# Kernel optimization log

Hardware: AMD Instinct MI355X
Metric: run time of the kernel (lower is better)

The kernel has to match this reference:

```python
import jax, jax.numpy as jnp
import numpy as np

EMBED_DIM = 1024
NUM_HEADS = 16
HEAD_DIM = EMBED_DIM // NUM_HEADS
SEQ = 2048
BSZ = 2


def setup_inputs() -> dict:
    key = jax.random.key(0)
    ks = jax.random.split(key, 12)
    f = jnp.float32
    query = jax.random.normal(ks[0], (SEQ, BSZ, EMBED_DIM), f)
    k_in = jax.random.normal(ks[1], (SEQ, BSZ, EMBED_DIM), f)
    v_in = jax.random.normal(ks[2], (SEQ, BSZ, EMBED_DIM), f)
    s = 0.02  # weight init scale
    q_w = jax.random.normal(ks[3], (EMBED_DIM, EMBED_DIM), f) * s
    q_b = jax.random.normal(ks[4], (EMBED_DIM,), f) * s
    k_w = jax.random.normal(ks[5], (EMBED_DIM, EMBED_DIM), f) * s
    k_b = jax.random.normal(ks[6], (EMBED_DIM,), f) * s
    v_w = jax.random.normal(ks[7], (EMBED_DIM, EMBED_DIM), f) * s
    v_b = jax.random.normal(ks[8], (EMBED_DIM,), f) * s
    o_w_mean = jax.random.normal(ks[9], (EMBED_DIM, EMBED_DIM), f) * s
    # lgstd ~ uniform(2*log(stdv), log(stdv)) with stdv = 1/sqrt(out+1)
    stdv = 1.0 / np.sqrt(EMBED_DIM + 1)
    o_w_lgstd = jax.random.uniform(ks[10], (EMBED_DIM, EMBED_DIM), f,
                                   2.0 * np.log(stdv), np.log(stdv))
    eps = jax.random.normal(ks[11], (EMBED_DIM, EMBED_DIM), f) * 1.5  # N(0, 1.5)
    return dict(query=query, key=k_in, value=v_in,
                q_w=q_w, q_b=q_b, k_w=k_w, k_b=k_b, v_w=v_w, v_b=v_b,
                o_w_mean=o_w_mean, o_w_lgstd=o_w_lgstd, eps=eps)


def reference(query, key, value, q_w, q_b, k_w, k_b, v_w, v_b,
              o_w_mean, o_w_lgstd, eps):
    tgt_len, bsz, embed_dim = query.shape
    scaling = HEAD_DIM ** -0.5
    # projections (F.linear: x @ W.T + b)
    q = (query @ q_w.T + q_b) * scaling          # [S,B,E]
    k = key @ k_w.T + k_b                        # [S,B,E]
    v = value @ v_w.T + v_b                      # [S,B,E]
    # [S,B,E] -> [B*H, S, hd]
    def split_heads(x, L):
        return x.reshape(L, bsz * NUM_HEADS, HEAD_DIM).transpose(1, 0, 2)
    q = split_heads(q, tgt_len)
    k = split_heads(k, key.shape[0])
    v = split_heads(v, value.shape[0])
    src_len = k.shape[1]
    scores = jnp.einsum('bqd,bkd->bqk', q, k)    # [B*H, S, S] (explicit O(n^2))
    attn = jax.nn.softmax(scores, axis=-1)
    ctx = jnp.einsum('bqk,bkd->bqd', attn, v)    # [B*H, S, hd]
    ctx = ctx.transpose(1, 0, 2).reshape(tgt_len, bsz, embed_dim)
    # Bayesian output projection: sampled weight (training mode), no bias
    o_w = o_w_mean + eps * jnp.exp(o_w_lgstd)
    out = ctx @ o_w.T                            # [S,B,E]
    avg_attn = attn.reshape(bsz, NUM_HEADS, tgt_len, src_len).sum(axis=1) / NUM_HEADS
    return out, avg_attn
```

## Files before the change

kernel.cpp:

```cpp
#include <hip/hip_runtime.h>

#define SQ 2048
#define BB 2
#define EE 1024
#define HH 16
#define DD 64
#define MM (SQ*BB)
#define NSLICE 4
#define KSLICE (SQ/NSLICE)
#define KT_IN (KSLICE/128)
#define LOG2E 1.44269504f

typedef _Float16 f16;
typedef _Float16 half8 __attribute__((ext_vector_type(8)));
typedef _Float16 half4 __attribute__((ext_vector_type(4)));
typedef float f32x4 __attribute__((ext_vector_type(4)));

static __device__ __forceinline__ f32x4 mfma16(half8 a, half8 b, f32x4 c) {
    return __builtin_amdgcn_mfma_f32_16x16x32_f16(a, b, c, 0, 0, 0);
}

static __device__ __forceinline__ void gload16(const f16* g, f16* l) {
    __builtin_amdgcn_global_load_lds(
        (const __attribute__((address_space(1))) unsigned int*)g,
        (__attribute__((address_space(3))) unsigned int*)l, 16, 0, 0);
}

__global__ void k_elem(const float* __restrict__ q_w, const float* __restrict__ k_w,
                       const float* __restrict__ v_w, const float* __restrict__ query,
                       const float* __restrict__ key, const float* __restrict__ value,
                       const float* __restrict__ owm, const float* __restrict__ owl,
                       const float* __restrict__ eps,
                       f16* qw16, f16* kw16, f16* vw16,
                       f16* xq16, f16* xk16, f16* xv16, f16* ow16)
{
    int y = blockIdx.y;
    size_t i = ((size_t)blockIdx.x * 256 + threadIdx.x) * 4;
    if (y < 3) {
        if (i >= (size_t)EE*EE) return;
        const float* s = (y==0) ? q_w : (y==1) ? k_w : v_w;
        f16* d = (y==0) ? qw16 : (y==1) ? kw16 : vw16;
        float4 v = *(const float4*)&s[i];
        half4 o = {(f16)v.x, (f16)v.y, (f16)v.z, (f16)v.w};
        *(half4*)&d[i] = o;
    } else if (y < 6) {
        const float* s = (y==3) ? query : (y==4) ? key : value;
        f16* d = (y==3) ? xq16 : (y==4) ? xk16 : xv16;
        float4 v = *(const float4*)&s[i];
        half4 o = {(f16)v.x, (f16)v.y, (f16)v.z, (f16)v.w};
        *(half4*)&d[i] = o;
    } else {
        if (i >= (size_t)EE*EE) return;
        float4 m = *(const float4*)&owm[i];
        float4 l = *(const float4*)&owl[i];
        float4 e = *(const float4*)&eps[i];
        half4 o = {(f16)(m.x + e.x * __expf(l.x)), (f16)(m.y + e.y * __expf(l.y)),
                   (f16)(m.z + e.z * __expf(l.z)), (f16)(m.w + e.w * __expf(l.w))};
        *(half4*)&ow16[i] = o;
    }
}

__device__ __forceinline__ void gemm_body(
    const f16* __restrict__ A, const f16* __restrict__ W,
    const float* __restrict__ bias, float scale, void* __restrict__ out, int mode)
{
    __shared__ f16 As[128*32];
    __shared__ f16 Bs[64*32];
    int t = threadIdx.x, lane = t & 63, w = t >> 6;
    int quad = lane >> 4, m16 = lane & 15;
    int wm = w >> 1, wn = w & 1;
    int gm0 = blockIdx.x * 128, gn0 = blockIdx.y * 64;
    int arow = lane >> 2, apch = lane & 3;
    f32x4 acc[4][2] = {};
    for (int kt = 0; kt < EE; kt += 32) {
        #pragma unroll
        for (int j = 0; j < 2; ++j) {
            int row = w*32 + j*16 + arow;
            int lch = apch ^ (row & 3);
            gload16(&A[(size_t)(gm0+row)*EE + kt + lch*8], &As[row*32 + apch*8]);
        }
        {
            int row = w*16 + arow;
            int lch = apch ^ (row & 3);
            gload16(&W[(size_t)(gn0+row)*EE + kt + lch*8], &Bs[row*32 + apch*8]);
        }
        __syncthreads();
        int cs = (quad ^ (m16 & 3)) * 8;
        half8 af[4], bf[2];
        #pragma unroll
        for (int i = 0; i < 4; ++i) af[i] = *(half8*)&As[(wm*64 + i*16 + m16)*32 + cs];
        #pragma unroll
        for (int j = 0; j < 2; ++j) bf[j] = *(half8*)&Bs[(wn*32 + j*16 + m16)*32 + cs];
        #pragma unroll
        for (int i = 0; i < 4; ++i)
            #pragma unroll
            for (int j = 0; j < 2; ++j)
                acc[i][j] = mfma16(af[i], bf[j], acc[i][j]);
        __syncthreads();
    }
    #pragma unroll
    for (int j = 0; j < 2; ++j) {
        int col = gn0 + wn*32 + j*16 + m16;
        float bb = bias ? bias[col] : 0.0f;
        #pragma unroll
        for (int i = 0; i < 4; ++i) {
            int r0 = gm0 + wm*64 + i*16 + quad*4;
            #pragma unroll
            for (int r = 0; r < 4; ++r) {
                float v = (acc[i][j][r] + bb) * scale;
                int m = r0 + r;
                if (mode == 2)      ((float*)out)[(size_t)m*EE + col] = v;
                else if (mode == 1) ((f16*)out)[((size_t)(m & 1)*EE + col)*SQ + (m >> 1)] = (f16)v;
                else                ((f16*)out)[(size_t)m*EE + col] = (f16)v;
            }
        }
    }
}

__global__ __launch_bounds__(256) void k_gemm_qkv(
    const f16* xq, const f16* qw, const float* qb,
    const f16* xk, const f16* kw, const float* kb,
    const f16* xv, const f16* vw, const float* vb,
    f16* Q16, f16* K16, f16* Vt16)
{
    int z = blockIdx.z;
    const f16* A = (z==0) ? xq : (z==1) ? xk : xv;
    const f16* W = (z==0) ? qw : (z==1) ? kw : vw;
    const float* bi = (z==0) ? qb : (z==1) ? kb : vb;
    float sc = (z==0) ? 0.125f * LOG2E : 1.0f;
    void* o = (z==0) ? (void*)Q16 : (z==1) ? (void*)K16 : (void*)Vt16;
    gemm_body(A, W, bi, sc, o, (z==2) ? 1 : 0);
}

__global__ __launch_bounds__(256) void k_gemm_o(const f16* A, const f16* W, float* out)
{
    gemm_body(A, W, nullptr, 1.0f, out, 2);
}

__global__ __launch_bounds__(256, 4) void k_attn_l(
    const f16* __restrict__ Q16, const f16* __restrict__ K16, float* __restrict__ lse2)
{
    __shared__ float red[4][64];
    const int t = threadIdx.x, lane = t & 63, w = t >> 6;
    const int quad = lane >> 4, m16 = lane & 15;
    const int q0 = blockIdx.x * 64, h = blockIdx.y, b = blockIdx.z;

    half8 bq[4][2];
    #pragma unroll
    for (int nt = 0; nt < 4; ++nt)
        #pragma unroll
        for (int dk = 0; dk < 2; ++dk)
            bq[nt][dk] = *(const half8*)&Q16[(size_t)((q0 + nt*16 + m16)*BB + b)*EE + h*DD + dk*32 + quad*8];

    float lsum[4] = {};
    for (int kt = 0; kt < 16; ++kt) {
        half8 ak[2][2];
        #pragma unroll
        for (int mt = 0; mt < 2; ++mt)
            #pragma unroll
            for (int dk = 0; dk < 2; ++dk)
                ak[mt][dk] = *(const half8*)&K16[(size_t)((kt*128 + w*32 + mt*16 + m16)*BB + b)*EE + h*DD + dk*32 + quad*8];
        #pragma unroll
        for (int mt = 0; mt < 2; ++mt)
            #pragma unroll
            for (int nt = 0; nt < 4; ++nt) {
                f32x4 s = {};
                s = mfma16(ak[mt][0], bq[nt][0], s);
                s = mfma16(ak[mt][1], bq[nt][1], s);
                lsum[nt] += __builtin_amdgcn_exp2f(s[0]) + __builtin_amdgcn_exp2f(s[1])
                          + __builtin_amdgcn_exp2f(s[2]) + __builtin_amdgcn_exp2f(s[3]);
            }
    }
    #pragma unroll
    for (int nt = 0; nt < 4; ++nt) {
        float v = lsum[nt];
        v += __shfl_xor(v, 16, 64);
        v += __shfl_xor(v, 32, 64);
        lsum[nt] = v;
    }
    if (quad == 0)
        #pragma unroll
        for (int nt = 0; nt < 4; ++nt) red[w][nt*16 + m16] = lsum[nt];
    __syncthreads();
    if (t < 64) {
        float v = red[0][t] + red[1][t] + red[2][t] + red[3][t];
        lse2[((size_t)b*HH + h)*SQ + q0 + t] = __log2f(v);
    }
}

__global__ __launch_bounds__(256, 2) void k_attn_main(
    const f16* __restrict__ Q16, const f16* __restrict__ K16, const f16* __restrict__ Vt16,
    const float* __restrict__ lse2, float* __restrict__ ctxp, float* __restrict__ avg_out)
{
    __shared__ f16 ps[2][32][136];
    __shared__ float csh[HH][32];
    const int t = threadIdx.x, lane = t & 63, w = t >> 6;
    const int quad = lane >> 4, m16 = lane & 15;
    const int q0 = blockIdx.x * 32, sl = blockIdx.y, b = blockIdx.z;
    const int ks0 = sl * KSLICE;

    for (int i = t; i < HH*32; i += 256) {
        int hh = i >> 5, qq = i & 31;
        csh[hh][qq] = lse2[((size_t)b*HH + hh)*SQ + q0 + qq];
    }
    __syncthreads();

    float avg_r[KT_IN][16] = {};

    for (int hp = 0; hp < 8; ++hp) {
        f32x4 acc[2][2] = {};
        for (int hh2 = 0; hh2 < 2; ++hh2) {
            const int h = hp*2 + hh2;
            half8 bq[2][2];
            #pragma unroll
            for (int nt = 0; nt < 2; ++nt)
                #pragma unroll
                for (int dk = 0; dk < 2; ++dk)
                    bq[nt][dk] = *(const half8*)&Q16[(size_t)((q0 + nt*16 + m16)*BB + b)*EE + h*DD + dk*32 + quad*8];
            const float c01[2] = { csh[h][m16], csh[h][16 + m16] };

            half8 ak[2][2][2], bv[2][4];
            #pragma unroll
            for (int mt = 0; mt < 2; ++mt)
                #pragma unroll
                for (int dk = 0; dk < 2; ++dk)
                    ak[0][mt][dk] = *(const half8*)&K16[(size_t)((ks0 + w*32 + mt*16 + m16)*BB + b)*EE + h*DD + dk*32 + quad*8];
            #pragma unroll
            for (int ks = 0; ks < 4; ++ks)
                bv[0][ks] = *(const half8*)&Vt16[((size_t)b*EE + h*DD + w*16 + m16)*SQ + ks0 + ks*32 + quad*8];

            #pragma unroll
            for (int kt = 0; kt < KT_IN; ++kt) {
                const int cur = kt & 1, nxt = cur ^ 1;
                if (kt + 1 < KT_IN) {
                    #pragma unroll
                    for (int mt = 0; mt < 2; ++mt)
                        #pragma unroll
                        for (int dk = 0; dk < 2; ++dk)
                            ak[nxt][mt][dk] = *(const half8*)&K16[(size_t)((ks0 + (kt+1)*128 + w*32 + mt*16 + m16)*BB + b)*EE + h*DD + dk*32 + quad*8];
                    #pragma unroll
                    for (int ks = 0; ks < 4; ++ks)
                        bv[nxt][ks] = *(const half8*)&Vt16[((size_t)b*EE + h*DD + w*16 + m16)*SQ + ks0 + (kt+1)*128 + ks*32 + quad*8];
                }
                #pragma unroll
                for (int mt = 0; mt < 2; ++mt)
                    #pragma unroll
                    for (int nt = 0; nt < 2; ++nt) {
                        f32x4 s = {};
                        s = mfma16(ak[cur][mt][0], bq[nt][0], s);
                        s = mfma16(ak[cur][mt][1], bq[nt][1], s);
                        half4 ph;
                        #pragma unroll
                        for (int r = 0; r < 4; ++r) {
                            float p = __builtin_amdgcn_exp2f(s[r] - c01[nt]);
                            avg_r[kt][mt*8 + nt*4 + r] += p;
                            ph[r] = (f16)p;
                        }
                        *(half4*)&ps[cur][nt*16 + m16][w*32 + mt*16 + quad*4] = ph;
                    }
                __syncthreads();
                #pragma unroll
                for (int qt = 0; qt < 2; ++qt) {
                    f32x4 c4 = acc[hh2][qt];
                    #pragma unroll
                    for (int ks = 0; ks < 4; ++ks) {
                        half8 ap = *(half8*)&ps[cur][qt*16 + m16][ks*32 + quad*8];
                        c4 = mfma16(ap, bv[cur][ks], c4);
                    }
                    acc[hh2][qt] = c4;
                }
            }
        }
        #pragma unroll
        for (int hh2 = 0; hh2 < 2; ++hh2)
            #pragma unroll
            for (int qt = 0; qt < 2; ++qt)
                #pragma unroll
                for (int r = 0; r < 4; ++r) {
                    int q = q0 + qt*16 + quad*4 + r;
                    ctxp[(size_t)sl*MM*EE + ((size_t)q*BB + b)*EE + (hp*2 + hh2)*DD + w*16 + m16] = acc[hh2][qt][r];
                }
    }
    #pragma unroll
    for (int kt = 0; kt < KT_IN; ++kt)
        #pragma unroll
        for (int mt = 0; mt < 2; ++mt)
            #pragma unroll
            for (int nt = 0; nt < 2; ++nt) {
                int q = q0 + nt*16 + m16;
                int k = ks0 + kt*128 + w*32 + mt*16 + quad*4;
                float4 v = { avg_r[kt][mt*8+nt*4+0]*(1.0f/HH), avg_r[kt][mt*8+nt*4+1]*(1.0f/HH),
                             avg_r[kt][mt*8+nt*4+2]*(1.0f/HH), avg_r[kt][mt*8+nt*4+3]*(1.0f/HH) };
                *(float4*)&avg_out[((size_t)b*SQ + q)*SQ + k] = v;
            }
}

__global__ void k_ctx_red(const float* __restrict__ ctxp, f16* __restrict__ ctx16) {
    size_t i = ((size_t)blockIdx.x * 256 + threadIdx.x) * 4;
    float4 s = *(const float4*)&ctxp[i];
    #pragma unroll
    for (int sl = 1; sl < NSLICE; ++sl) {
        float4 v = *(const float4*)&ctxp[(size_t)sl*MM*EE + i];
        s.x += v.x; s.y += v.y; s.z += v.z; s.w += v.w;
    }
    half4 o = {(f16)s.x, (f16)s.y, (f16)s.z, (f16)s.w};
    *(half4*)&ctx16[i] = o;
}

extern "C" void kernel_launch(void* const* d_in, const int* in_sizes, int n_in,
                              void* d_out, int out_size, void* d_ws, size_t ws_size,
                              hipStream_t stream) {
    const float* query    = (const float*)d_in[0];
    const float* key      = (const float*)d_in[1];
    const float* value    = (const float*)d_in[2];
    const float* q_w      = (const float*)d_in[3];
    const float* q_b      = (const float*)d_in[4];
    const float* k_w      = (const float*)d_in[5];
    const float* k_b      = (const float*)d_in[6];
    const float* v_w      = (const float*)d_in[7];
    const float* v_b      = (const float*)d_in[8];
    const float* o_w_mean = (const float*)d_in[9];
    const float* o_w_lgstd= (const float*)d_in[10];
    const float* eps      = (const float*)d_in[11];
    float* out = (float*)d_out;
    float* avg = out + (size_t)MM * EE;

    const size_t EWN = (size_t)EE*EE;
    const size_t XWN = (size_t)MM*EE;
    f16* qw16  = (f16*)d_ws;
    f16* kw16  = qw16 + EWN;
    f16* vw16  = kw16 + EWN;
    f16* ow16  = vw16 + EWN;
    f16* Q16   = ow16 + EWN;
    f16* K16   = Q16  + XWN;
    f16* Vt16  = K16  + XWN;
    f16* ctx16 = Vt16 + XWN;
    float* lse2 = (float*)(ctx16 + XWN);
    f16* xq16  = (f16*)(lse2 + (size_t)BB*HH*SQ);
    f16* xk16  = xq16 + XWN;
    f16* xv16  = xk16 + XWN;
    float* ctxp = (float*)xq16;

    k_elem<<<dim3(XWN/1024, 7), 256, 0, stream>>>(q_w, k_w, v_w, query, key, value,
        o_w_mean, o_w_lgstd, eps, qw16, kw16, vw16, xq16, xk16, xv16, ow16);

    k_gemm_qkv<<<dim3(MM/128, EE/64, 3), 256, 0, stream>>>(
        xq16, qw16, q_b, xk16, kw16, k_b, xv16, vw16, v_b, Q16, K16, Vt16);

    k_attn_l   <<<dim3(SQ/64, HH, BB), 256, 0, stream>>>(Q16, K16, lse2);
    k_attn_main<<<dim3(SQ/32, NSLICE, BB), 256, 0, stream>>>(Q16, K16, Vt16, lse2, ctxp, avg);
    k_ctx_red  <<<XWN/1024, 256, 0, stream>>>(ctxp, ctx16);

    k_gemm_o<<<dim3(MM/128, EE/64), 256, 0, stream>>>(ctx16, ow16, out);
}
```

Before: 392.4 us.

## Split attention into separate avg-weights and context kernels, enlarge GEMM tiles

Replaces the fused attention kernel, which split keys into four slices and needed a partial-context reduction pass, with two kernels. One computes the head-averaged attention weights per (q,k) tile, and the other computes the context per head directly into fp16, with no split-K partials. This removes the fp32 partial-context writes and the reduction kernel, at the cost of computing QK^T and exp twice. The GEMM tile is also widened from 128x64 to 128x128, with a launch-bounds occupancy hint added.

```diff
diff --git a/kernel.cpp b/kernel.cpp
--- a/kernel.cpp
+++ b/kernel.cpp
@@ -6,9 +6,6 @@
 #define HH 16
 #define DD 64
 #define MM (SQ*BB)
-#define NSLICE 4
-#define KSLICE (SQ/NSLICE)
-#define KT_IN (KSLICE/128)
 #define LOG2E 1.44269504f
 
 typedef _Float16 f16;
@@ -65,42 +62,38 @@
     const float* __restrict__ bias, float scale, void* __restrict__ out, int mode)
 {
     __shared__ f16 As[128*32];
-    __shared__ f16 Bs[64*32];
+    __shared__ f16 Bs[128*32];
     int t = threadIdx.x, lane = t & 63, w = t >> 6;
     int quad = lane >> 4, m16 = lane & 15;
     int wm = w >> 1, wn = w & 1;
-    int gm0 = blockIdx.x * 128, gn0 = blockIdx.y * 64;
-    int arow = lane >> 2, apch = lane & 3;
-    f32x4 acc[4][2] = {};
+    int gm0 = blockIdx.x * 128, gn0 = blockIdx.y * 128;
+    f32x4 acc[4][4] = {};
     for (int kt = 0; kt < EE; kt += 32) {
         #pragma unroll
-        for (int j = 0; j < 2; ++j) {
-            int row = w*32 + j*16 + arow;
-            int lch = apch ^ (row & 3);
-            gload16(&A[(size_t)(gm0+row)*EE + kt + lch*8], &As[row*32 + apch*8]);
-        }
-        {
-            int row = w*16 + arow;
-            int lch = apch ^ (row & 3);
-            gload16(&W[(size_t)(gn0+row)*EE + kt + lch*8], &Bs[row*32 + apch*8]);
+        for (int i = 0; i < 2; ++i) {
+            int c = t + i * 256;
+            int row = c >> 2, pch = c & 3;
+            int lch = pch ^ (row & 3);
+            gload16(&A[(size_t)(gm0+row)*EE + kt + lch*8], &As[row*32 + pch*8]);
+            gload16(&W[(size_t)(gn0+row)*EE + kt + lch*8], &Bs[row*32 + pch*8]);
         }
         __syncthreads();
         int cs = (quad ^ (m16 & 3)) * 8;
-        half8 af[4], bf[2];
+        half8 af[4], bf[4];
         #pragma unroll
         for (int i = 0; i < 4; ++i) af[i] = *(half8*)&As[(wm*64 + i*16 + m16)*32 + cs];
         #pragma unroll
-        for (int j = 0; j < 2; ++j) bf[j] = *(half8*)&Bs[(wn*32 + j*16 + m16)*32 + cs];
+        for (int j = 0; j < 4; ++j) bf[j] = *(half8*)&Bs[(wn*64 + j*16 + m16)*32 + cs];
         #pragma unroll
         for (int i = 0; i < 4; ++i)
             #pragma unroll
-            for (int j = 0; j < 2; ++j)
+            for (int j = 0; j < 4; ++j)
                 acc[i][j] = mfma16(af[i], bf[j], acc[i][j]);
         __syncthreads();
     }
     #pragma unroll
-    for (int j = 0; j < 2; ++j) {
-        int col = gn0 + wn*32 + j*16 + m16;
+    for (int j = 0; j < 4; ++j) {
+        int col = gn0 + wn*64 + j*16 + m16;
         float bb = bias ? bias[col] : 0.0f;
         #pragma unroll
         for (int i = 0; i < 4; ++i) {
@@ -117,7 +110,7 @@
     }
 }
 
-__global__ __launch_bounds__(256) void k_gemm_qkv(
+__global__ __launch_bounds__(256, 3) void k_gemm_qkv(
     const f16* xq, const f16* qw, const float* qb,
     const f16* xk, const f16* kw, const float* kb,
     const f16* xv, const f16* vw, const float* vb,
@@ -132,12 +125,12 @@
     gemm_body(A, W, bi, sc, o, (z==2) ? 1 : 0);
 }
 
-__global__ __launch_bounds__(256) void k_gemm_o(const f16* A, const f16* W, float* out)
+__global__ __launch_bounds__(256, 3) void k_gemm_o(const f16* A, const f16* W, float* out)
 {
     gemm_body(A, W, nullptr, 1.0f, out, 2);
 }
 
-__global__ __launch_bounds__(256, 4) void k_attn_l(
+__global__ __launch_bounds__(256, 4) void k_lse(
     const f16* __restrict__ Q16, const f16* __restrict__ K16, float* __restrict__ lse2)
 {
     __shared__ float red[4][64];
@@ -188,123 +181,105 @@
     }
 }
 
-__global__ __launch_bounds__(256, 2) void k_attn_main(
-    const f16* __restrict__ Q16, const f16* __restrict__ K16, const f16* __restrict__ Vt16,
-    const float* __restrict__ lse2, float* __restrict__ ctxp, float* __restrict__ avg_out)
-{
-    __shared__ f16 ps[2][32][136];
-    __shared__ float csh[HH][32];
+__global__ __launch_bounds__(256, 2) void k_avg(
+    const f16* __restrict__ Q16, const f16* __restrict__ K16,
+    const float* __restrict__ lse2, float* __restrict__ avg_out)
+{
     const int t = threadIdx.x, lane = t & 63, w = t >> 6;
     const int quad = lane >> 4, m16 = lane & 15;
-    const int q0 = blockIdx.x * 32, sl = blockIdx.y, b = blockIdx.z;
-    const int ks0 = sl * KSLICE;
-
-    for (int i = t; i < HH*32; i += 256) {
-        int hh = i >> 5, qq = i & 31;
-        csh[hh][qq] = lse2[((size_t)b*HH + hh)*SQ + q0 + qq];
-    }
-    __syncthreads();
-
-    float avg_r[KT_IN][16] = {};
-
-    for (int hp = 0; hp < 8; ++hp) {
-        f32x4 acc[2][2] = {};
-        for (int hh2 = 0; hh2 < 2; ++hh2) {
-            const int h = hp*2 + hh2;
-            half8 bq[2][2];
-            #pragma unroll
-            for (int nt = 0; nt < 2; ++nt)
+    const int q0 = blockIdx.x * 64, k0 = blockIdx.y * 256, b = blockIdx.z;
+    const int kw = k0 + w * 64;
+
+    float avg_r[4][4][4] = {};
+    for (int h = 0; h < HH; ++h) {
+        float c[4];
+        #pragma unroll
+        for (int nt = 0; nt < 4; ++nt)
+            c[nt] = lse2[((size_t)b*HH + h)*SQ + q0 + nt*16 + m16];
+        half8 bq[4][2], ak[4][2];
+        #pragma unroll
+        for (int nt = 0; nt < 4; ++nt)
+            #pragma unroll
+            for (int dk = 0; dk < 2; ++dk)
+                bq[nt][dk] = *(const half8*)&Q16[(size_t)((q0 + nt*16 + m16)*BB + b)*EE + h*DD + dk*32 + quad*8];
+        #pragma unroll
+        for (int mt = 0; mt < 4; ++mt)
+            #pragma unroll
+            for (int dk = 0; dk < 2; ++dk)
+                ak[mt][dk] = *(const half8*)&K16[(size_t)((kw + mt*16 + m16)*BB + b)*EE + h*DD + dk*32 + quad*8];
+        #pragma unroll
+        for (int mt = 0; mt < 4; ++mt)
+            #pragma unroll
+            for (int nt = 0; nt < 4; ++nt) {
+                f32x4 s = {};
+                s = mfma16(ak[mt][0], bq[nt][0], s);
+                s = mfma16(ak[mt][1], bq[nt][1], s);
                 #pragma unroll
-                for (int dk = 0; dk < 2; ++dk)
-                    bq[nt][dk] = *(const half8*)&Q16[(size_t)((q0 + nt*16 + m16)*BB + b)*EE + h*DD + dk*32 + quad*8];
-            const float c01[2] = { csh[h][m16], csh[h][16 + m16] };
-
-            half8 ak[2][2][2], bv[2][4];
-            #pragma unroll
-            for (int mt = 0; mt < 2; ++mt)
-                #pragma unroll
-                for (int dk = 0; dk < 2; ++dk)
-                    ak[0][mt][dk] = *(const half8*)&K16[(size_t)((ks0 + w*32 + mt*16 + m16)*BB + b)*EE + h*DD + dk*32 + quad*8];
-            #pragma unroll
-            for (int ks = 0; ks < 4; ++ks)
-                bv[0][ks] = *(const half8*)&Vt16[((size_t)b*EE + h*DD + w*16 + m16)*SQ + ks0 + ks*32 + quad*8];
-
-            #pragma unroll
-            for (int kt = 0; kt < KT_IN; ++kt) {
-                const int cur = kt & 1, nxt = cur ^ 1;
-                if (kt + 1 < KT_IN) {
-                    #pragma unroll
-                    for (int mt = 0; mt < 2; ++mt)
-                        #pragma unroll
-                        for (int dk = 0; dk < 2; ++dk)
-                            ak[nxt][mt][dk] = *(const half8*)&K16[(size_t)((ks0 + (kt+1)*128 + w*32 + mt*16 + m16)*BB + b)*EE + h*DD + dk*32 + quad*8];
-                    #pragma unroll
-                    for (int ks = 0; ks < 4; ++ks)
-                        bv[nxt][ks] = *(const half8*)&Vt16[((size_t)b*EE + h*DD + w*16 + m16)*SQ + ks0 + (kt+1)*128 + ks*32 + quad*8];
-                }
-                #pragma unroll
-                for (int mt = 0; mt < 2; ++mt)
-                    #pragma unroll
-                    for (int nt = 0; nt < 2; ++nt) {
-                        f32x4 s = {};
-                        s = mfma16(ak[cur][mt][0], bq[nt][0], s);
-                        s = mfma16(ak[cur][mt][1], bq[nt][1], s);
-                        half4 ph;
-                        #pragma unroll
-                        for (int r = 0; r < 4; ++r) {
-                            float p = __builtin_amdgcn_exp2f(s[r] - c01[nt]);
-                            avg_r[kt][mt*8 + nt*4 + r] += p;
-                            ph[r] = (f16)p;
-                        }
-                        *(half4*)&ps[cur][nt*16 + m16][w*32 + mt*16 + quad*4] = ph;
-                    }
-                __syncthreads();
-                #pragma unroll
-                for (int qt = 0; qt < 2; ++qt) {
-                    f32x4 c4 = acc[hh2][qt];
-                    #pragma unroll
-                    for (int ks = 0; ks < 4; ++ks) {
-                        half8 ap = *(half8*)&ps[cur][qt*16 + m16][ks*32 + quad*8];
-                        c4 = mfma16(ap, bv[cur][ks], c4);
-                    }
-                    acc[hh2][qt] = c4;
-                }
+                for (int r = 0; r < 4; ++r)
+                    avg_r[mt][nt][r] += __builtin_amdgcn_exp2f(s[r] - c[nt]);
             }
-        }
-        #pragma unroll
-        for (int hh2 = 0; hh2 < 2; ++hh2)
-            #pragma unroll
-            for (int qt = 0; qt < 2; ++qt)
-                #pragma unroll
-                for (int r = 0; r < 4; ++r) {
-                    int q = q0 + qt*16 + quad*4 + r;
-                    ctxp[(size_t)sl*MM*EE + ((size_t)q*BB + b)*EE + (hp*2 + hh2)*DD + w*16 + m16] = acc[hh2][qt][r];
-                }
-    }
-    #pragma unroll
-    for (int kt = 0; kt < KT_IN; ++kt)
-        #pragma unroll
-        for (int mt = 0; mt < 2; ++mt)
-            #pragma unroll
-            for (int nt = 0; nt < 2; ++nt) {
-                int q = q0 + nt*16 + m16;
-                int k = ks0 + kt*128 + w*32 + mt*16 + quad*4;
-                float4 v = { avg_r[kt][mt*8+nt*4+0]*(1.0f/HH), avg_r[kt][mt*8+nt*4+1]*(1.0f/HH),
-                             avg_r[kt][mt*8+nt*4+2]*(1.0f/HH), avg_r[kt][mt*8+nt*4+3]*(1.0f/HH) };
-                *(float4*)&avg_out[((size_t)b*SQ + q)*SQ + k] = v;
+    }
+    #pragma unroll
+    for (int mt = 0; mt < 4; ++mt)
+        #pragma unroll
+        for (int nt = 0; nt < 4; ++nt) {
+            int q = q0 + nt*16 + m16;
+            int k = kw + mt*16 + quad*4;
+            float4 v = { avg_r[mt][nt][0]*(1.0f/HH), avg_r[mt][nt][1]*(1.0f/HH),
+                         avg_r[mt][nt][2]*(1.0f/HH), avg_r[mt][nt][3]*(1.0f/HH) };
+            *(float4*)&avg_out[((size_t)b*SQ + q)*SQ + k] = v;
+        }
+}
+
+__global__ __launch_bounds__(256, 2) void k_ctx(
+    const f16* __restrict__ Q16, const f16* __restrict__ K16, const f16* __restrict__ Vt16,
+    const float* __restrict__ lse2, f16* __restrict__ ctx16)
+{
+    __shared__ f16 psb[4][16*136];
+    const int t = threadIdx.x, lane = t & 63, w = t >> 6;
+    const int quad = lane >> 4, m16 = lane & 15;
+    const int qw = blockIdx.x * 64 + w * 16;
+    const int h = blockIdx.y, b = blockIdx.z;
+    f16* ps = psb[w];
+
+    half8 bq[2];
+    #pragma unroll
+    for (int dk = 0; dk < 2; ++dk)
+        bq[dk] = *(const half8*)&Q16[(size_t)((qw + m16)*BB + b)*EE + h*DD + dk*32 + quad*8];
+    const float c = lse2[((size_t)b*HH + h)*SQ + qw + m16];
+
+    f32x4 acc[4] = {};
+    for (int kt = 0; kt < SQ/128; ++kt) {
+        #pragma unroll
+        for (int mt = 0; mt < 8; ++mt) {
+            half8 ak0 = *(const half8*)&K16[(size_t)((kt*128 + mt*16 + m16)*BB + b)*EE + h*DD + quad*8];
+            half8 ak1 = *(const half8*)&K16[(size_t)((kt*128 + mt*16 + m16)*BB + b)*EE + h*DD + 32 + quad*8];
+            f32x4 s = {};
+            s = mfma16(ak0, bq[0], s);
+            s = mfma16(ak1, bq[1], s);
+            half4 ph;
+            #pragma unroll
+            for (int r = 0; r < 4; ++r)
+                ph[r] = (f16)__builtin_amdgcn_exp2f(s[r] - c);
+            *(half4*)&ps[m16*136 + mt*16 + quad*4] = ph;
+        }
+        #pragma unroll
+        for (int ks = 0; ks < 4; ++ks) {
+            half8 ap = *(half8*)&ps[m16*136 + ks*32 + quad*8];
+            #pragma unroll
+            for (int dt = 0; dt < 4; ++dt) {
+                half8 bv = *(const half8*)&Vt16[((size_t)b*EE + h*DD + dt*16 + m16)*SQ + kt*128 + ks*32 + quad*8];
+                acc[dt] = mfma16(ap, bv, acc[dt]);
             }
-}
-
-__global__ void k_ctx_red(const float* __restrict__ ctxp, f16* __restrict__ ctx16) {
-    size_t i = ((size_t)blockIdx.x * 256 + threadIdx.x) * 4;
-    float4 s = *(const float4*)&ctxp[i];
-    #pragma unroll
-    for (int sl = 1; sl < NSLICE; ++sl) {
-        float4 v = *(const float4*)&ctxp[(size_t)sl*MM*EE + i];
-        s.x += v.x; s.y += v.y; s.z += v.z; s.w += v.w;
-    }
-    half4 o = {(f16)s.x, (f16)s.y, (f16)s.z, (f16)s.w};
-    *(half4*)&ctx16[i] = o;
+        }
+    }
+    #pragma unroll
+    for (int dt = 0; dt < 4; ++dt)
+        #pragma unroll
+        for (int r = 0; r < 4; ++r) {
+            int q = qw + quad*4 + r;
+            ctx16[(size_t)(q*BB + b)*EE + h*DD + dt*16 + m16] = (f16)acc[dt][r];
+        }
 }
 
 extern "C" void kernel_launch(void* const* d_in, const int* in_sizes, int n_in,
@@ -339,17 +314,16 @@
     f16* xq16  = (f16*)(lse2 + (size_t)BB*HH*SQ);
     f16* xk16  = xq16 + XWN;
     f16* xv16  = xk16 + XWN;
-    float* ctxp = (float*)xq16;
 
     k_elem<<<dim3(XWN/1024, 7), 256, 0, stream>>>(q_w, k_w, v_w, query, key, value,
         o_w_mean, o_w_lgstd, eps, qw16, kw16, vw16, xq16, xk16, xv16, ow16);
 
-    k_gemm_qkv<<<dim3(MM/128, EE/64, 3), 256, 0, stream>>>(
+    k_gemm_qkv<<<dim3(MM/128, EE/128, 3), 256, 0, stream>>>(
         xq16, qw16, q_b, xk16, kw16, k_b, xv16, vw16, v_b, Q16, K16, Vt16);
 
-    k_attn_l   <<<dim3(SQ/64, HH, BB), 256, 0, stream>>>(Q16, K16, lse2);
-    k_attn_main<<<dim3(SQ/32, NSLICE, BB), 256, 0, stream>>>(Q16, K16, Vt16, lse2, ctxp, avg);
-    k_ctx_red  <<<XWN/1024, 256, 0, stream>>>(ctxp, ctx16);
-
-    k_gemm_o<<<dim3(MM/128, EE/64), 256, 0, stream>>>(ctx16, ow16, out);
-}
+    k_lse<<<dim3(SQ/64, HH, BB), 256, 0, stream>>>(Q16, K16, lse2);
+    k_avg<<<dim3(SQ/64, SQ/256, BB), 256, 0, stream>>>(Q16, K16, lse2, avg);
+    k_ctx<<<dim3(SQ/64, HH, BB), 256, 0, stream>>>(Q16, K16, Vt16, lse2, ctx16);
+
+    k_gemm_o<<<dim3(MM/128, EE/128), 256, 0, stream>>>(ctx16, ow16, out);
+}
```

Result: slower. 519.9 us (+32.5%).
